# Performance work log

Hardware: AMD Instinct MI355X
Metric: run time of the kernel (lower is better)

The kernel has to match this reference:

```python
import jax, jax.numpy as jnp
import numpy as np

H = 128        # hidden_size
E = 128        # embedding_size
D = 2 * H      # num_directions * hidden_size
B = 512        # batch
T = 100        # n_cities == max_time_steps
MID = 100
STD = 0.1


def _p(k, shape):
    return STD * jax.random.normal(k, shape, dtype=jnp.float32)


def setup_inputs():
    ks = jax.random.split(jax.random.key(0), 22)
    return {
        "inputs": jax.random.normal(ks[0], (B, T, 2), dtype=jnp.float32),
        "W_embed": _p(ks[1], (E, 2)),
        "enc_Wih_f": _p(ks[2], (4 * H, E)),
        "enc_Whh_f": _p(ks[3], (4 * H, H)),
        "enc_b_f": _p(ks[4], (4 * H,)),
        "enc_Wih_b": _p(ks[5], (4 * H, E)),
        "enc_Whh_b": _p(ks[6], (4 * H, H)),
        "enc_b_b": _p(ks[7], (4 * H,)),
        "W_ref": _p(ks[8], (D, D)),
        "W_q": _p(ks[9], (D, D)),
        "v_w": _p(ks[10], (D,)),
        "v_b": _p(ks[11], (1,)),
        "proc_Wih_f": _p(ks[12], (4 * H, D)),
        "proc_Whh_f": _p(ks[13], (4 * H, H)),
        "proc_b_f": _p(ks[14], (4 * H,)),
        "proc_Wih_b": _p(ks[15], (4 * H, D)),
        "proc_Whh_b": _p(ks[16], (4 * H, H)),
        "proc_b_b": _p(ks[17], (4 * H,)),
        "W1": _p(ks[18], (MID, D)),
        "b1": _p(ks[19], (MID,)),
        "W2": _p(ks[20], (1, MID)),
        "b2": _p(ks[21], (1,)),
    }


def _cell(x, h, c, Wih, Whh, b):
    # PyTorch LSTM gate order: i, f, g, o
    gates = x @ Wih.T + h @ Whh.T + b
    i, f, g, o = jnp.split(gates, 4, axis=-1)
    c2 = jax.nn.sigmoid(f) * c + jax.nn.sigmoid(i) * jnp.tanh(g)
    h2 = jax.nn.sigmoid(o) * jnp.tanh(c2)
    return h2, c2


def _lstm_dir(xs, Wih, Whh, b):
    # xs: [T, B, in] -> (hs [T,B,H], h_last [B,H], c_last [B,H])
    bsz = xs.shape[1]
    h0 = jnp.zeros((bsz, H), xs.dtype)

    def step(carry, x):
        h, c = carry
        h, c = _cell(x, h, c, Wih, Whh, b)
        return (h, c), h

    (h, c), hs = jax.lax.scan(step, (h0, h0), xs)
    return hs, h, c


def _forward(inputs, W_embed, enc_Wih_f, enc_Whh_f, enc_b_f, enc_Wih_b, enc_Whh_b,
             enc_b_b, W_ref, W_q, v_w, v_b, proc_Wih_f, proc_Whh_f, proc_b_f,
             proc_Wih_b, proc_Whh_b, proc_b_b, W1, b1, W2, b2, remat=False):
    bsz, city, _ = inputs.shape
    emb = inputs @ W_embed.T                      # [B, T, E]
    xs = emb.transpose(1, 0, 2)                   # [T, B, E]
    hs_f, hf, cf = _lstm_dir(xs, enc_Wih_f, enc_Whh_f, enc_b_f)
    hs_b, hb, cb = _lstm_dir(xs[::-1], enc_Wih_b, enc_Whh_b, enc_b_b)
    enc = jnp.concatenate([hs_f, hs_b[::-1]], axis=-1).transpose(1, 0, 2)  # [B, T, D]
    ref = enc @ W_ref.T                           # loop-invariant W_ref(Enc): [B, T, D]

    def step(carry, _):
        pin, shf, scf, shb, scb = carry
        # bidirectional LSTM over a length-1 sequence = two independent cells
        shf, scf = _cell(pin, shf, scf, proc_Wih_f, proc_Whh_f, proc_b_f)
        shb, scb = _cell(pin, shb, scb, proc_Wih_b, proc_Whh_b, proc_b_b)
        pout = jnp.concatenate([shf, shb], axis=-1)              # [B, D]
        scores = jnp.tanh(ref + (pout @ W_q.T)[:, None, :]) @ v_w + v_b[0]  # [B, T]
        attn = jax.nn.softmax(scores, axis=1)
        pin = jnp.einsum('bt,btd->bd', attn, enc)                # glimpse
        return (pin, shf, scf, shb, scb), pout

    if remat:
        step = jax.checkpoint(step)

    pin0 = jnp.zeros((bsz, D), inputs.dtype)
    _, pouts = jax.lax.scan(step, (pin0, hf, cf, hb, cb), None, length=city)
    pout = pouts[-1]                              # processor_output of last step
    hidden = jax.nn.relu(pout @ W1.T + b1)
    return jnp.squeeze(hidden @ W2.T + b2)        # [B]


def reference(inputs, W_embed, enc_Wih_f, enc_Whh_f, enc_b_f, enc_Wih_b, enc_Whh_b,
              enc_b_b, W_ref, W_q, v_w, v_b, proc_Wih_f, proc_Whh_f, proc_b_f,
              proc_Wih_b, proc_Whh_b, proc_b_b, W1, b1, W2, b2):
    return _forward(inputs, W_embed, enc_Wih_f, enc_Whh_f, enc_b_f, enc_Wih_b,
                    enc_Whh_b, enc_b_b, W_ref, W_q, v_w, v_b, proc_Wih_f,
                    proc_Whh_f, proc_b_f, proc_Wih_b, proc_Whh_b, proc_b_b,
                    W1, b1, W2, b2)
```

## Files before the change

### kernel.cpp

```cpp
#include <hip/hip_runtime.h>


constexpr int kH = 128, kE = 128, kD = 256, kB = 512, kT = 100, kG = 512, kMID = 100;

typedef _Float16 half2_t __attribute__((ext_vector_type(2)));

constexpr size_t WS_ENCH  = 0;
constexpr size_t WS_REFTH = WS_ENCH  + (size_t)kB * kT * kD/2;
constexpr size_t WS_EW2   = WS_REFTH + (size_t)kB * kD * kT/2;
constexpr size_t WS_ECG   = WS_EW2   + 65536;
constexpr size_t WS_PW2   = WS_ECG   + 4096;
constexpr size_t WS_PB    = WS_PW2   + 196608;
constexpr size_t WS_WQ2   = WS_PB    + 1024;
constexpr size_t WS_WREFT = WS_WQ2   + 32768;
constexpr size_t WS_HST   = WS_WREFT + (size_t)kD * kD;
constexpr size_t WS_POUT  = WS_HST   + (size_t)4 * kB * kH;

__device__ __forceinline__ float rcpf(float x) { return __builtin_amdgcn_rcpf(x); }
__device__ __forceinline__ float sigf(float x) { return rcpf(1.0f + __expf(-x)); }
__device__ __forceinline__ float tanhf_(float x) {
    float t = __expf(2.0f * x);
    return 1.0f - 2.0f * rcpf(1.0f + t);
}
__device__ __forceinline__ float fdot2(half2_t a, half2_t b, float c) {
#if __has_builtin(__builtin_amdgcn_fdot2)
    return __builtin_amdgcn_fdot2(a, b, c, false);
#else
    return c + (float)a.x * (float)b.x + (float)a.y * (float)b.y;
#endif
}

__global__ void k_prep_ec(const float* __restrict__ Wih_f, const float* __restrict__ Wih_b,
                          const float* __restrict__ b_f, const float* __restrict__ b_b,
                          const float* __restrict__ Wemb, float* __restrict__ ws) {
    int id = blockIdx.x * 256 + threadIdx.x;
    int dir = id >> 9, j = id & 511;
    const float* Wih = dir ? Wih_b : Wih_f;
    const float* bb  = dir ? b_b   : b_f;
    float c0 = 0.f, c1 = 0.f;
    for (int e = 0; e < kE; ++e) {
        float w = Wih[j * kE + e];
        c0 += w * Wemb[e * 2 + 0];
        c1 += w * Wemb[e * 2 + 1];
    }
    float* ecg = ws + WS_ECG + (size_t)id * 4;
    ecg[0] = c0; ecg[1] = c1; ecg[2] = bb[j]; ecg[3] = 0.f;
}

__global__ void k_prep_tr(const float* __restrict__ eWhh_f, const float* __restrict__ eWhh_b,
                          const float* __restrict__ pWih_f, const float* __restrict__ pWih_b,
                          const float* __restrict__ pWhh_f, const float* __restrict__ pWhh_b,
                          const float* __restrict__ pb_f, const float* __restrict__ pb_b,
                          const float* __restrict__ Wq, const float* __restrict__ Wref,
                          float* __restrict__ ws) {
    int id = blockIdx.x * 256 + threadIdx.x;
    if (id < 65536) {
        int dir = id >> 15, rem = id & 32767, kp = rem >> 9, j = rem & 511;
        const float* W = dir ? eWhh_b : eWhh_f;
        half2_t v = {(_Float16)W[j * kH + 2 * kp], (_Float16)W[j * kH + 2 * kp + 1]};
        ((half2_t*)(ws + WS_EW2))[id] = v;
        return;
    }
    id -= 65536;
    if (id < 196608) {
        int kp = id >> 10, j = id & 1023;
        int k0 = 2 * kp, k1 = 2 * kp + 1;
        float a, b;
        if (k0 < 256) {
            a = (j < 512) ? pWih_f[j * kD + k0] : pWih_b[(j - 512) * kD + k0];
            b = (j < 512) ? pWih_f[j * kD + k1] : pWih_b[(j - 512) * kD + k1];
        } else {
            a = (j < 512) ? pWhh_f[j * kH + (k0 - 256)] : pWhh_b[(j - 512) * kH + (k0 - 256)];
            b = (j < 512) ? pWhh_f[j * kH + (k1 - 256)] : pWhh_b[(j - 512) * kH + (k1 - 256)];
        }
        half2_t v = {(_Float16)a, (_Float16)b};
        ((half2_t*)(ws + WS_PW2))[id] = v;
        return;
    }
    id -= 196608;
    if (id < 1024) {
        ws[WS_PB + id] = (id < 512) ? pb_f[id] : pb_b[id - 512];
        return;
    }
    id -= 1024;
    if (id < 32768) {
        int kp = id >> 8, n = id & 255;
        half2_t v = {(_Float16)Wq[n * kD + 2 * kp], (_Float16)Wq[n * kD + 2 * kp + 1]};
        ((half2_t*)(ws + WS_WQ2))[id] = v;
        return;
    }
    id -= 32768;
    if (id < 65536) {
        int k = id >> 8, n = id & 255;
        ws[WS_WREFT + id] = Wref[n * kD + k];
        return;
    }
}

__global__ __launch_bounds__(512) void k_encoder(const float* __restrict__ inp,
                                                 float* __restrict__ ws) {
    const int dir = blockIdx.x & 1;
    const int b0  = (blockIdx.x >> 1) * 4;
    const int tid = threadIdx.x;
    const int jq  = tid & 127;
    const int kg  = tid >> 7;
    __shared__ __align__(16) half2_t shT2[64][4];
    __shared__ float scs[4][kH];
    __shared__ __align__(16) float uniE[4 * 4 * 512];
    __shared__ __align__(16) float4 secg[512];
    __shared__ float sx[4][2];
    if (tid < 256) ((float*)shT2)[tid] = 0.f;
    if (tid < 512) scs[tid >> 7][tid & 127] = 0.f;
    secg[tid] = *(const float4*)(ws + WS_ECG + (size_t)(dir * 512 + tid) * 4);
    const float4* EW2f4 = (const float4*)(ws + WS_EW2) + (size_t)dir * 64 * 128;
    _Float16* ench = (_Float16*)(ws + WS_ENCH);
    float* hst = ws + WS_HST;
    float4* uniE4 = (float4*)uniE;
    __syncthreads();
    for (int s = 0; s < kT; ++s) {
        const int t = dir ? (kT - 1 - s) : s;
        if (tid < 8) { int r = tid >> 1, c = tid & 1; sx[r][c] = inp[((size_t)(b0 + r) * kT + t) * 2 + c]; }
        {
            float aa[16];
            #pragma unroll
            for (int i = 0; i < 16; ++i) aa[i] = 0.f;
            #pragma unroll 8
            for (int kk = 0; kk < 16; ++kk) {
                int kp = kg * 16 + kk;
                float4 wraw = EW2f4[kp * 128 + jq];
                float4 xraw = *(const float4*)&shT2[kp][0];
                const half2_t* wp = (const half2_t*)&wraw;
                const half2_t* xp = (const half2_t*)&xraw;
                #pragma unroll
                for (int j = 0; j < 4; ++j)
                    #pragma unroll
                    for (int r = 0; r < 4; ++r)
                        aa[j * 4 + r] = fdot2(wp[j], xp[r], aa[j * 4 + r]);
            }
            #pragma unroll
            for (int r = 0; r < 4; ++r)
                uniE4[(kg * 4 + r) * 128 + jq] = make_float4(aa[0*4+r], aa[1*4+r], aa[2*4+r], aa[3*4+r]);
        }
        __syncthreads();
        {
            const int r = tid >> 7, k = tid & 127;
            float4 c0 = secg[k], c1 = secg[128 + k], c2 = secg[256 + k], c3 = secg[384 + k];
            float x0 = sx[r][0], x1 = sx[r][1];
            float gi = c0.z + x0 * c0.x + x1 * c0.y;
            float gf = c1.z + x0 * c1.x + x1 * c1.y;
            float gg = c2.z + x0 * c2.x + x1 * c2.y;
            float go = c3.z + x0 * c3.x + x1 * c3.y;
            #pragma unroll
            for (int g4 = 0; g4 < 4; ++g4) {
                const float* u = &uniE[(g4 * 4 + r) * 512];
                gi += u[k]; gf += u[k + 128]; gg += u[k + 256]; go += u[k + 384];
            }
            float cc = sigf(gf) * scs[r][k] + sigf(gi) * tanhf_(gg);
            float hh = sigf(go) * tanhf_(cc);
            scs[r][k] = cc;
            ((_Float16*)shT2)[((k >> 1) * 4 + r) * 2 + (k & 1)] = (_Float16)hh;
            ench[((size_t)(b0 + r) * kT + t) * kD + dir * kH + k] = (_Float16)hh;
            if (s == kT - 1) {
                hst[(size_t)(dir * 2 + 0) * kB * kH + (size_t)(b0 + r) * kH + k] = hh;
                hst[(size_t)(dir * 2 + 1) * kB * kH + (size_t)(b0 + r) * kH + k] = cc;
            }
        }
        __syncthreads();
    }
}

__global__ __launch_bounds__(256) void k_refgemm(float* __restrict__ ws) {
    const int tid = threadIdx.x;
    const int m0 = blockIdx.x * 20;
    const int b = m0 / kT, t0 = m0 % kT;
    __shared__ float se[20][kD];
    __shared__ float so[20][257];
    const _Float16* ench = (const _Float16*)(ws + WS_ENCH);
    const float* WrT = ws + WS_WREFT;
    _Float16* refTh = (_Float16*)(ws + WS_REFTH);
    #pragma unroll
    for (int i = 0; i < 20; ++i) se[i][tid] = (float)ench[(size_t)(m0 + i) * kD + tid];
    __syncthreads();
    float acc[20];
    #pragma unroll
    for (int r = 0; r < 20; ++r) acc[r] = 0.f;
    #pragma unroll 2
    for (int k = 0; k < kD; ++k) {
        float w = WrT[k * kD + tid];
        #pragma unroll
        for (int r = 0; r < 20; ++r) acc[r] += se[r][k] * w;
    }
    #pragma unroll
    for (int r = 0; r < 20; ++r) so[r][tid] = acc[r];
    __syncthreads();
    #pragma unroll
    for (int i = 0; i < 20; ++i) {
        int idx = i * 256 + tid;
        int d = idx / 20, tt = idx - d * 20;
        refTh[(size_t)b * kD * kT + d * kT + t0 + tt] = (_Float16)so[tt][d];
    }
}

__global__ __launch_bounds__(1024) void k_process(const float* __restrict__ vw,
                                                  const float* __restrict__ vb,
                                                  float* __restrict__ ws) {
    const int tid = threadIdx.x;
    const int b0 = blockIdx.x * 2;
    __shared__ __align__(16) half2_t xh2[2][192][2];
    __shared__ float pc[2][2][kH];
    __shared__ float hfp[2][2][kH];
    __shared__ __align__(16) float uni[8192];
    __shared__ float qv[2][kD];
    __shared__ float at[2][128];
    __shared__ float vwS[kD];
    __shared__ float sbias[1024];
    const float* PB   = ws + WS_PB;
    const _Float16* refTh = (const _Float16*)(ws + WS_REFTH);
    const _Float16* ench  = (const _Float16*)(ws + WS_ENCH);
    const float* hst  = ws + WS_HST;
    const float4* PW2f4 = (const float4*)(ws + WS_PW2);
    const float*  WQ2f  = ws + WS_WQ2;
    _Float16* xf = (_Float16*)xh2;
    if (tid < 512) {
        int zjh = tid >> 8, zkp = (tid >> 1) & 127, zr = tid & 1;
        ((float*)xh2)[(zjh * 192 + zkp) * 2 + zr] = 0.f;
    }
    if (tid < 512) {
        int r = tid >> 8, dirk = tid & 255, dir = dirk >> 7, k = dirk & 127;
        float hv = hst[(size_t)(dir * 2 + 0) * kB * kH + (size_t)(b0 + r) * kH + k];
        pc[dir][r][k]  = hst[(size_t)(dir * 2 + 1) * kB * kH + (size_t)(b0 + r) * kH + k];
        hfp[dir][r][k] = hv;
        xf[((dir * 192 + 128 + (k >> 1)) * 2 + r) * 2 + (k & 1)] = (_Float16)hv;
    }
    if (tid < kD) vwS[tid] = vw[tid];
    sbias[tid] = PB[tid];
    const float vbias = vb[0];
    const int jq = tid & 255;
    const int kg = tid >> 8;
    const int jh = (jq >= 128);
    float4* uni4 = (float4*)uni;
    __syncthreads();

    for (int step = 0; step < kT; ++step) {
        {
            float a00=0,a01=0,a02=0,a03=0, a10=0,a11=0,a12=0,a13=0;
            #pragma unroll 8
            for (int kk = 0; kk < 48; ++kk) {
                int kp = kg * 48 + kk;
                float4 wraw = PW2f4[(size_t)kp * 256 + jq];
                float2 xraw = *(const float2*)&xh2[jh][kp][0];
                const half2_t* wp = (const half2_t*)&wraw;
                const half2_t* xp = (const half2_t*)&xraw;
                a00 = fdot2(wp[0], xp[0], a00); a01 = fdot2(wp[1], xp[0], a01);
                a02 = fdot2(wp[2], xp[0], a02); a03 = fdot2(wp[3], xp[0], a03);
                a10 = fdot2(wp[0], xp[1], a10); a11 = fdot2(wp[1], xp[1], a11);
                a12 = fdot2(wp[2], xp[1], a12); a13 = fdot2(wp[3], xp[1], a13);
            }
            uni4[(kg * 2 + 0) * 256 + jq] = make_float4(a00,a01,a02,a03);
            uni4[(kg * 2 + 1) * 256 + jq] = make_float4(a10,a11,a12,a13);
        }
        __syncthreads();
        if (tid < 512) {
            int r = tid >> 8, dirk = tid & 255, dir = dirk >> 7, k = dirk & 127;
            int base = dir * 512;
            int j0 = base + k, j1 = base + 128 + k, j2 = base + 256 + k, j3 = base + 384 + k;
            float gi = sbias[j0], gf = sbias[j1], gg = sbias[j2], go = sbias[j3];
            #pragma unroll
            for (int g4 = 0; g4 < 4; ++g4) {
                const float* u = &uni[(g4 * 2 + r) * 1024];
                gi += u[j0]; gf += u[j1]; gg += u[j2]; go += u[j3];
            }
            float cc = sigf(gf) * pc[dir][r][k] + sigf(gi) * tanhf_(gg);
            float hh = sigf(go) * tanhf_(cc);
            pc[dir][r][k] = cc; hfp[dir][r][k] = hh;
            xf[((dir * 192 + 128 + (k >> 1)) * 2 + r) * 2 + (k & 1)] = (_Float16)hh;
        }
        __syncthreads();
        if (step < kT - 1) {
            {
                int n = tid & 255, kh = tid >> 8;
                float q0 = 0.f, q1 = 0.f;
                #pragma unroll 8
                for (int i = 0; i < 32; ++i) {
                    int kp = kh * 32 + i;
                    int dir = kp >> 6, lkp = kp & 63;
                    float wr = WQ2f[kp * 256 + n];
                    float2 xraw = *(const float2*)&xh2[dir][128 + lkp][0];
                    const half2_t* xp = (const half2_t*)&xraw;
                    half2_t w = *(const half2_t*)&wr;
                    q0 = fdot2(w, xp[0], q0);
                    q1 = fdot2(w, xp[1], q1);
                }
                uni[(kh * 2 + 0) * 256 + n] = q0;
                uni[(kh * 2 + 1) * 256 + n] = q1;
            }
            __syncthreads();
            if (tid < 512) {
                int r = tid >> 8, n = tid & 255;
                float q = 0.f;
                #pragma unroll
                for (int kh = 0; kh < 4; ++kh) q += uni[(kh * 2 + r) * 256 + n];
                qv[r][n] = q;
            }
            __syncthreads();
            if (tid < 800) {
                int r = tid / 400, rem = tid - r * 400;
                int dg = rem / 100, t = rem - dg * 100;
                const _Float16* rrow = refTh + ((size_t)(b0 + r) * kD + dg * 64) * kT + t;
                float acc = 0.f;
                #pragma unroll 8
                for (int i = 0; i < 64; ++i) {
                    int d = dg * 64 + i;
                    float rv = (float)rrow[(size_t)i * kT];
                    acc += vwS[d] * tanhf_(rv + qv[r][d]);
                }
                uni[(r * 4 + dg) * 100 + t] = acc;
            }
            __syncthreads();
            {
                int wv = tid >> 6, l = tid & 63;
                if (wv < 2) {
                    int r = wv;
                    float s1 = vbias + uni[(r*4+0)*100 + l] + uni[(r*4+1)*100 + l]
                                     + uni[(r*4+2)*100 + l] + uni[(r*4+3)*100 + l];
                    float s2 = -3.0e38f;
                    if (l + 64 < kT)
                        s2 = vbias + uni[(r*4+0)*100 + l+64] + uni[(r*4+1)*100 + l+64]
                                   + uni[(r*4+2)*100 + l+64] + uni[(r*4+3)*100 + l+64];
                    float m = fmaxf(s1, s2);
                    #pragma unroll
                    for (int off = 32; off > 0; off >>= 1) m = fmaxf(m, __shfl_xor(m, off));
                    float e1 = __expf(s1 - m);
                    float e2 = (l + 64 < kT) ? __expf(s2 - m) : 0.f;
                    float ssum = e1 + e2;
                    #pragma unroll
                    for (int off = 32; off > 0; off >>= 1) ssum += __shfl_xor(ssum, off);
                    float inv = rcpf(ssum);
                    at[r][l] = e1 * inv;
                    at[r][l + 64] = e2 * inv;
                }
            }
            __syncthreads();
            {
                int dp = tid & 127, r = (tid >> 7) & 1, th = tid >> 8;
                const half2_t* erow = (const half2_t*)(ench + ((size_t)(b0 + r) * kT + th * 25) * kD) + dp;
                float a0 = 0.f, a1 = 0.f;
                #pragma unroll 5
                for (int i = 0; i < 25; ++i) {
                    half2_t e = erow[(size_t)i * (kD / 2)];
                    float w = at[r][th * 25 + i];
                    a0 += w * (float)e.x;
                    a1 += w * (float)e.y;
                }
                uni[(th * 2 + r) * 256 + 2 * dp]     = a0;
                uni[(th * 2 + r) * 256 + 2 * dp + 1] = a1;
            }
            __syncthreads();
            if (tid < 512) {
                int r = tid >> 8, d = tid & 255;
                float v = 0.f;
                #pragma unroll
                for (int th = 0; th < 4; ++th) v += uni[(th * 2 + r) * 256 + d];
                _Float16 hv = (_Float16)v;
                xf[((0 * 192 + (d >> 1)) * 2 + r) * 2 + (d & 1)] = hv;
                xf[((1 * 192 + (d >> 1)) * 2 + r) * 2 + (d & 1)] = hv;
            }
            __syncthreads();
        }
    }
    float* pout = ws + WS_POUT;
    if (tid < 512) {
        int r = tid >> 8, d = tid & 255;
        pout[(size_t)(b0 + r) * kD + d] = (d < 128) ? hfp[0][r][d] : hfp[1][r][d - 128];
    }
}

__global__ __launch_bounds__(128) void k_mlp(const float* __restrict__ W1, const float* __restrict__ b1,
                                             const float* __restrict__ W2, const float* __restrict__ b2,
                                             const float* __restrict__ ws, float* __restrict__ out) {
    const int tid = threadIdx.x;
    const int b0 = blockIdx.x * 4;
    __shared__ float sp[4][kD];
    __shared__ float hid[4][kMID];
    const float* pout = ws + WS_POUT;
    #pragma unroll
    for (int i = 0; i < 8; ++i) {
        int f = i * 128 + tid;
        int r = f >> 8, k = f & 255;
        sp[r][k] = pout[(size_t)(b0 + r) * kD + k];
    }
    __syncthreads();
    if (tid < kMID) {
        int m = tid;
        #pragma unroll
        for (int r = 0; r < 4; ++r) {
            float acc = b1[m];
            for (int k = 0; k < kD; ++k) acc += sp[r][k] * W1[m * kD + k];
            hid[r][m] = fmaxf(acc, 0.f);
        }
    }
    __syncthreads();
    if (tid < 4) {
        float acc = b2[0];
        for (int m = 0; m < kMID; ++m) acc += hid[tid][m] * W2[m];
        out[b0 + tid] = acc;
    }
}

extern "C" void kernel_launch(void* const* d_in, const int* in_sizes, int n_in,
                              void* d_out, int out_size, void* d_ws, size_t ws_size,
                              hipStream_t stream) {
    (void)in_sizes; (void)n_in; (void)out_size; (void)ws_size;
    const float* inp    = (const float*)d_in[0];
    const float* Wemb   = (const float*)d_in[1];
    const float* eWih_f = (const float*)d_in[2];
    const float* eWhh_f = (const float*)d_in[3];
    const float* eb_f   = (const float*)d_in[4];
    const float* eWih_b = (const float*)d_in[5];
    const float* eWhh_b = (const float*)d_in[6];
    const float* eb_b   = (const float*)d_in[7];
    const float* Wref   = (const float*)d_in[8];
    const float* Wq     = (const float*)d_in[9];
    const float* vw     = (const float*)d_in[10];
    const float* vb     = (const float*)d_in[11];
    const float* pWih_f = (const float*)d_in[12];
    const float* pWhh_f = (const float*)d_in[13];
    const float* pb_f   = (const float*)d_in[14];
    const float* pWih_b = (const float*)d_in[15];
    const float* pWhh_b = (const float*)d_in[16];
    const float* pb_b   = (const float*)d_in[17];
    const float* W1     = (const float*)d_in[18];
    const float* b1     = (const float*)d_in[19];
    const float* W2     = (const float*)d_in[20];
    const float* b2     = (const float*)d_in[21];
    float* ws  = (float*)d_ws;
    float* out = (float*)d_out;

    k_prep_ec<<<4, 256, 0, stream>>>(eWih_f, eWih_b, eb_f, eb_b, Wemb, ws);
    k_prep_tr<<<1412, 256, 0, stream>>>(eWhh_f, eWhh_b, pWih_f, pWih_b,
                                        pWhh_f, pWhh_b, pb_f, pb_b, Wq, Wref, ws);
    k_encoder<<<256, 512, 0, stream>>>(inp, ws);
    k_refgemm<<<2560, 256, 0, stream>>>(ws);
    k_process<<<256, 1024, 0, stream>>>(vw, vb, ws);
    k_mlp<<<128, 128, 0, stream>>>(W1, b1, W2, b2, ws, out);
}
```

Before: 2.280 ms.

## Cache recurrent LSTM weights in registers and simplify the glimpse reduction

The encoder now loads its per-thread recurrent weight slice into registers once, instead of re-reading it from global memory every time step. The processor kernel does the same for the recurrent (hidden-to-hidden) part of its gate weights and keeps streaming the input-weight part. The glimpse computation drops its 4-way split over time and one shared-memory reduction plus barrier, so 512 threads each loop over all 100 steps. Launch bounds now request minimum occupancy, which may force register spills, and the glimpse loop is longer per thread with fewer threads active.

New measurement: 5.146 ms. 126% more time.

```diff
diff --git a/kernel.cpp b/kernel.cpp
--- a/kernel.cpp
+++ b/kernel.cpp
@@ -97,8 +97,8 @@
     }
 }
 
-__global__ __launch_bounds__(512) void k_encoder(const float* __restrict__ inp,
-                                                 float* __restrict__ ws) {
+__global__ __launch_bounds__(512, 2) void k_encoder(const float* __restrict__ inp,
+                                                    float* __restrict__ ws) {
     const int dir = blockIdx.x & 1;
     const int b0  = (blockIdx.x >> 1) * 4;
     const int tid = threadIdx.x;
@@ -116,6 +116,9 @@
     _Float16* ench = (_Float16*)(ws + WS_ENCH);
     float* hst = ws + WS_HST;
     float4* uniE4 = (float4*)uniE;
+    float4 wregE[16];
+    #pragma unroll
+    for (int i = 0; i < 16; ++i) wregE[i] = EW2f4[(kg * 16 + i) * 128 + jq];
     __syncthreads();
     for (int s = 0; s < kT; ++s) {
         const int t = dir ? (kT - 1 - s) : s;
@@ -124,12 +127,11 @@
             float aa[16];
             #pragma unroll
             for (int i = 0; i < 16; ++i) aa[i] = 0.f;
-            #pragma unroll 8
+            #pragma unroll
             for (int kk = 0; kk < 16; ++kk) {
                 int kp = kg * 16 + kk;
-                float4 wraw = EW2f4[kp * 128 + jq];
                 float4 xraw = *(const float4*)&shT2[kp][0];
-                const half2_t* wp = (const half2_t*)&wraw;
+                const half2_t* wp = (const half2_t*)&wregE[kk];
                 const half2_t* xp = (const half2_t*)&xraw;
                 #pragma unroll
                 for (int j = 0; j < 4; ++j)
@@ -201,9 +203,9 @@
     }
 }
 
-__global__ __launch_bounds__(1024) void k_process(const float* __restrict__ vw,
-                                                  const float* __restrict__ vb,
-                                                  float* __restrict__ ws) {
+__global__ __launch_bounds__(1024, 4) void k_process(const float* __restrict__ vw,
+                                                     const float* __restrict__ vb,
+                                                     float* __restrict__ ws) {
     const int tid = threadIdx.x;
     const int b0 = blockIdx.x * 2;
     __shared__ __align__(16) half2_t xh2[2][192][2];
@@ -239,17 +241,32 @@
     const int kg = tid >> 8;
     const int jh = (jq >= 128);
     float4* uni4 = (float4*)uni;
+    float4 wreg[16];
+    #pragma unroll
+    for (int i = 0; i < 16; ++i)
+        wreg[i] = PW2f4[(size_t)(128 + kg * 16 + i) * 256 + jq];
     __syncthreads();
 
     for (int step = 0; step < kT; ++step) {
         {
             float a00=0,a01=0,a02=0,a03=0, a10=0,a11=0,a12=0,a13=0;
             #pragma unroll 8
-            for (int kk = 0; kk < 48; ++kk) {
-                int kp = kg * 48 + kk;
+            for (int kk = 0; kk < 32; ++kk) {
+                int kp = kg * 32 + kk;
                 float4 wraw = PW2f4[(size_t)kp * 256 + jq];
                 float2 xraw = *(const float2*)&xh2[jh][kp][0];
                 const half2_t* wp = (const half2_t*)&wraw;
+                const half2_t* xp = (const half2_t*)&xraw;
+                a00 = fdot2(wp[0], xp[0], a00); a01 = fdot2(wp[1], xp[0], a01);
+                a02 = fdot2(wp[2], xp[0], a02); a03 = fdot2(wp[3], xp[0], a03);
+                a10 = fdot2(wp[0], xp[1], a10); a11 = fdot2(wp[1], xp[1], a11);
+                a12 = fdot2(wp[2], xp[1], a12); a13 = fdot2(wp[3], xp[1], a13);
+            }
+            #pragma unroll
+            for (int i = 0; i < 16; ++i) {
+                int kp = 128 + kg * 16 + i;
+                float2 xraw = *(const float2*)&xh2[jh][kp][0];
+                const half2_t* wp = (const half2_t*)&wreg[i];
                 const half2_t* xp = (const half2_t*)&xraw;
                 a00 = fdot2(wp[0], xp[0], a00); a01 = fdot2(wp[1], xp[0], a01);
                 a02 = fdot2(wp[2], xp[0], a02); a03 = fdot2(wp[3], xp[0], a03);
@@ -341,27 +358,14 @@
                 }
             }
             __syncthreads();
-            {
-                int dp = tid & 127, r = (tid >> 7) & 1, th = tid >> 8;
-                const half2_t* erow = (const half2_t*)(ench + ((size_t)(b0 + r) * kT + th * 25) * kD) + dp;
-                float a0 = 0.f, a1 = 0.f;
-                #pragma unroll 5
-                for (int i = 0; i < 25; ++i) {
-                    half2_t e = erow[(size_t)i * (kD / 2)];
-                    float w = at[r][th * 25 + i];
-                    a0 += w * (float)e.x;
-                    a1 += w * (float)e.y;
-                }
-                uni[(th * 2 + r) * 256 + 2 * dp]     = a0;
-                uni[(th * 2 + r) * 256 + 2 * dp + 1] = a1;
-            }
-            __syncthreads();
             if (tid < 512) {
                 int r = tid >> 8, d = tid & 255;
-                float v = 0.f;
-                #pragma unroll
-                for (int th = 0; th < 4; ++th) v += uni[(th * 2 + r) * 256 + d];
-                _Float16 hv = (_Float16)v;
+                const _Float16* erow = ench + (size_t)(b0 + r) * kT * kD + d;
+                float acc = 0.f;
+                #pragma unroll 4
+                for (int t = 0; t < kT; ++t)
+                    acc += at[r][t] * (float)erow[(size_t)t * kD];
+                _Float16 hv = (_Float16)acc;
                 xf[((0 * 192 + (d >> 1)) * 2 + r) * 2 + (d & 1)] = hv;
                 xf[((1 * 192 + (d >> 1)) * 2 + r) * 2 + (d & 1)] = hv;
             }
```
